# Kernel optimization log

Hardware: AMD Instinct MI355X
Metric: run time of the kernel (lower is better)

## Reference

```python
import jax, jax.numpy as jnp
import numpy as np

H = 768          # hidden_size
V = 512          # vocab_size
NUM_OPS = 64
N_INT = 2        # num_internal_ops
D = 13           # tree depth; complete binary tree
N_NODES = (1 << (D + 1)) - 1  # 16383, level-major layout: level d occupies [2^d-1, 2^(d+1)-1)
TEMP = 3.0


def setup_inputs() -> dict:
    key = jax.random.key(0)
    ks = jax.random.split(key, 24)
    s = 0.02
    nrm = lambda k, shp: jax.random.normal(k, shp, dtype=jnp.float32) * s
    return {
        "ids": jax.random.randint(ks[0], (N_NODES,), 0, V, dtype=jnp.int32),
        "mask": jax.random.randint(ks[1], (N_NODES, NUM_OPS), 0, 2, dtype=jnp.int32),
        # binary Tree-LSTM (N=2), Tai et al. N-ary formulation
        "Wb_iou": nrm(ks[2], (V, 3 * H)), "Ub_iou": nrm(ks[3], (2, H, 3 * H)), "bb_iou": jnp.zeros((3 * H,), jnp.float32),
        "Wb_f": nrm(ks[4], (V, H)), "Ub_f": nrm(ks[5], (2, 2, H, H)), "bb_f": jnp.ones((H,), jnp.float32),
        # ternary Tree-LSTM (N=3)
        "Wt_iou": nrm(ks[6], (V, 3 * H)), "Ut_iou": nrm(ks[7], (3, H, 3 * H)), "bt_iou": jnp.zeros((3 * H,), jnp.float32),
        "Wt_f": nrm(ks[8], (V, H)), "Ut_f": nrm(ks[9], (3, 3, H, H)), "bt_f": jnp.ones((H,), jnp.float32),
        # FFN(H,H,H,n_layers=1): Linear->ReLU->Linear
        "ffn_W1": nrm(ks[10], (H, H)), "ffn_b1": jnp.zeros((H,), jnp.float32),
        "ffn_W2": nrm(ks[11], (H, H)), "ffn_b2": jnp.zeros((H,), jnp.float32),
        # actor heads
        "hl_W": nrm(ks[12], (H, 2)), "hl_b": jnp.zeros((2,), jnp.float32),
        "int_W": nrm(ks[13], (H, N_INT)), "int_b": jnp.zeros((N_INT,), jnp.float32),
        "act_W": nrm(ks[14], (H, NUM_OPS)), "act_b": jnp.zeros((NUM_OPS,), jnp.float32),
    }


def _cell(x_iou, x_f, hc, cc, U_iou, b_iou, U_f, b_f):
    """Batched N-ary Tree-LSTM cell. hc, cc: (n, K, H)."""
    iou = x_iou + jnp.einsum('nkh,kho->no', hc, U_iou) + b_iou
    i, o, g = jnp.split(iou, 3, axis=-1)
    i = jax.nn.sigmoid(i); o = jax.nn.sigmoid(o); g = jnp.tanh(g)
    # per-child forget gate mixes all children hiddens
    f = jax.nn.sigmoid(x_f[:, None, :] + jnp.einsum('nlh,klho->nko', hc, U_f) + b_f)
    c = i * g + jnp.sum(f * cc, axis=1)
    h = o * jnp.tanh(c)
    return h, c


def reference(ids, mask,
              Wb_iou, Ub_iou, bb_iou, Wb_f, Ub_f, bb_f,
              Wt_iou, Ut_iou, bt_iou, Wt_f, Ut_f, bt_f,
              ffn_W1, ffn_b1, ffn_W2, ffn_b2,
              hl_W, hl_b, int_W, int_b, act_W, act_b):
    dt = Wb_iou.dtype
    # ---- apply_binary_lstm: bottom-up, batched per tree level ----
    h_lv = [None] * (D + 1)
    c_lv = [None] * (D + 1)
    for d in range(D, -1, -1):
        n = 1 << d
        off = n - 1
        lid = ids[off:off + n]
        if d == D:  # leaves: missing children -> zero hidden/cell (self.tz)
            hc = jnp.zeros((n, 2, H), dt); cc = jnp.zeros((n, 2, H), dt)
        else:
            hc = h_lv[d + 1].reshape(n, 2, H)
            cc = c_lv[d + 1].reshape(n, 2, H)
        h_lv[d], c_lv[d] = _cell(Wb_iou[lid], Wb_f[lid], hc, cc, Ub_iou, bb_iou, Ub_f, bb_f)
    # ---- internal op 1: apply_ternary_lstm(depth=0) at every node, batched ----
    # uses (own h, child-a h, child-b h); leaves get all zeros (a is None branch)
    h3_parts = []
    for d in range(D + 1):
        n = 1 << d
        off = n - 1
        lid = ids[off:off + n]
        if d == D:
            hc = jnp.zeros((n, 3, H), dt); cc = jnp.zeros((n, 3, H), dt)
        else:
            hc = jnp.concatenate([h_lv[d][:, None, :], h_lv[d + 1].reshape(n, 2, H)], axis=1)
            cc = jnp.concatenate([c_lv[d][:, None, :], c_lv[d + 1].reshape(n, 2, H)], axis=1)
        h3, _ = _cell(Wt_iou[lid], Wt_f[lid], hc, cc, Ut_iou, bt_iou, Ut_f, bt_f)
        h3_parts.append(h3)
    h = jnp.concatenate(h3_parts, axis=0)  # [N_NODES, H], level-major
    # ---- internal op 0: apply_ffn ----
    h = jax.nn.relu(h @ ffn_W1 + ffn_b1) @ ffn_W2 + ffn_b2
    # ---- policy heads (temperature softmaxes, masked actor) ----
    hl = jax.nn.softmax((h @ hl_W + hl_b) / TEMP, axis=-1)
    il = jax.nn.softmax((h @ int_W + int_b) / TEMP, axis=-1)
    mf = mask.astype(dt)
    lin = (h @ act_W + act_b) * mf                       # F.linear with mask-zeroed W, b
    logits = jnp.where(mf > 0, lin, jnp.asarray(-1e30, dt))  # validity_mask.log() + lin
    ap = jax.nn.softmax(logits / TEMP, axis=-1)
    return jnp.concatenate([hl, il, ap], axis=-1)  # [N_NODES, 2 + N_INT + NUM_OPS]
```

## Files before the change

kernel.cpp:

```cpp
#include <hip/hip_runtime.h>
#include <hip/hip_bf16.h>

#define HD 768
#define N_NODES 16383
#define NLEAF_OFF 8191
#define NHF 12582144
#define TEMP 3.0f

using bf16 = __hip_bfloat16;
typedef __attribute__((ext_vector_type(8))) short bf16x8;
typedef __attribute__((ext_vector_type(4))) float f32x4;

__device__ __forceinline__ float sigm(float x) { return 1.0f / (1.0f + __expf(-x)); }
__device__ __forceinline__ float b2f(bf16 v)   { return __bfloat162float(v); }
__device__ __forceinline__ bf16  f2b(float v)  { return __float2bfloat16(v); }

__device__ __forceinline__ void gload16(const void* g, void* l) {
    __builtin_amdgcn_global_load_lds(
        (const __attribute__((address_space(1))) unsigned int*)g,
        (__attribute__((address_space(3))) unsigned int*)l, 16, 0, 0);
}

#define T1SZ 5898240
#define T2SZ 10616832
#define WSZ  589824

__global__ __launch_bounds__(256) void tconv_k(
    const float* __restrict__ Ub_iou, const float* __restrict__ Ub_f,
    const float* __restrict__ Ut_iou, const float* __restrict__ Ut_f,
    const float* __restrict__ ffn_W1,
    bf16* __restrict__ BT1, bf16* __restrict__ BT2, bf16* __restrict__ W1T)
{
    int t = blockIdx.x;
    const float* src; bf16* dst; int C, S, kt, nt;
    if (t < 3456) {
        src = Ub_iou; dst = BT1; C = 2304; S = 1536;
        kt = t % 48; nt = t / 48;
    } else if (t < 5760) {
        int u = t - 3456; int piece = u / 576; u -= piece * 576;
        int kk = piece >> 1, l = piece & 1;
        src = Ub_f + (size_t)(kk * 2 + l) * WSZ;
        dst = BT1 + (size_t)(2304 + kk * 768) * 1536 + l * 768;
        C = 768; S = 1536; kt = u % 24; nt = u / 24;
    } else if (t < 10944) {
        int u = t - 5760;
        src = Ut_iou; dst = BT2; C = 2304; S = 2304;
        kt = u % 72; nt = u / 72;
    } else if (t < 16128) {
        int u = t - 10944; int piece = u / 576; u -= piece * 576;
        int kk = piece / 3, l = piece - kk * 3;
        src = Ut_f + (size_t)(kk * 3 + l) * WSZ;
        dst = BT2 + (size_t)(2304 + kk * 768) * 2304 + l * 768;
        C = 768; S = 2304; kt = u % 24; nt = u / 24;
    } else {
        int u = t - 16128;
        src = ffn_W1; dst = W1T; C = 768; S = 768;
        kt = u % 24; nt = u / 24;
    }
    int k0 = kt * 32, n0 = nt * 32;

    __shared__ float tl[32][33];
    int rr = threadIdx.x >> 5, c = threadIdx.x & 31;
#pragma unroll
    for (int r = 0; r < 32; r += 8)
        tl[rr + r][c] = src[(size_t)(k0 + rr + r) * C + n0 + c];
    __syncthreads();
#pragma unroll
    for (int r = 0; r < 32; r += 8)
        dst[(size_t)(n0 + rr + r) * S + k0 + c] = f2b(tl[c][rr + r]);
}

#define HSZ2 98304
__global__ __launch_bounds__(256) void misc_k(
    const float* __restrict__ hlW, const float* __restrict__ intW,
    const float* __restrict__ actW, const float* __restrict__ W2,
    bf16* __restrict__ WhT, bf16* __restrict__ W2b)
{
    int idx = blockIdx.x * 256 + threadIdx.x;
    if (idx < HSZ2) {
        int n = idx / 768, j = idx - n * 768;
        float v = 0.f;
        if (n < 2)       v = hlW[(size_t)j * 2 + n];
        else if (n < 4)  v = intW[(size_t)j * 2 + (n - 2)];
        else if (n < 68) v = actW[(size_t)j * 64 + (n - 4)];
        WhT[idx] = f2b(v);
    } else if (idx < HSZ2 + WSZ) {
        int i2 = idx - HSZ2;
        W2b[i2] = f2b(W2[i2]);
    }
}

__global__ __launch_bounds__(128) void bck_k(
    const float* __restrict__ b2,
    const float* __restrict__ hlW, const float* __restrict__ hlb,
    const float* __restrict__ intW, const float* __restrict__ intb,
    const float* __restrict__ actW, const float* __restrict__ actb,
    float* __restrict__ bc)
{
    int n = threadIdx.x;
    float s = 0.f;
    for (int j = 0; j < 768; ++j) {
        float wh = 0.f;
        if (n < 2)       wh = hlW[(size_t)j * 2 + n];
        else if (n < 4)  wh = intW[(size_t)j * 2 + (n - 2)];
        else if (n < 68) wh = actW[(size_t)j * 64 + (n - 4)];
        s = fmaf(b2[j], wh, s);
    }
    float hb = 0.f;
    if (n < 2)       hb = hlb[n];
    else if (n < 4)  hb = intb[n - 2];
    else if (n < 68) hb = actb[n - 4];
    bc[n] = s + hb;
}

__global__ __launch_bounds__(256) void vocab_k(
    const float* __restrict__ Wb, const float* __restrict__ bb,
    const float* __restrict__ Wt, const float* __restrict__ bt,
    bf16* __restrict__ Vh, bf16* __restrict__ Vc, bf16* __restrict__ Vh3)
{
    int idx = blockIdx.x * 256 + threadIdx.x;
    if (idx >= 512 * HD) return;
    int id = idx / HD, j = idx - id * HD;
    const float* w = Wb + (size_t)id * 3 * HD;
    float iv = sigm(w[j] + bb[j]);
    float ov = sigm(w[HD + j] + bb[HD + j]);
    float gv = tanhf(w[2 * HD + j] + bb[2 * HD + j]);
    float c = iv * gv;
    Vh[idx] = f2b(ov * tanhf(c));
    Vc[idx] = f2b(c);

    const float* w2 = Wt + (size_t)id * 3 * HD;
    float iv2 = sigm(w2[j] + bt[j]);
    float ov2 = sigm(w2[HD + j] + bt[HD + j]);
    float gv2 = tanhf(w2[2 * HD + j] + bt[2 * HD + j]);
    float c2 = iv2 * gv2;
    Vh3[idx] = f2b(ov2 * tanhf(c2));
}

__global__ __launch_bounds__(256) void lscat_k(
    const int* __restrict__ ids,
    const bf16* __restrict__ Vh, const bf16* __restrict__ Vc,
    const bf16* __restrict__ Vh3,
    bf16* __restrict__ h_all, bf16* __restrict__ c_all, bf16* __restrict__ h3_all)
{
    int idx = blockIdx.x * 256 + threadIdx.x;
    if (idx >= 8192 * 96) return;
    int i = idx / 96, j8 = (idx - i * 96) * 8;
    int g = NLEAF_OFF + i;
    size_t so = (size_t)ids[g] * HD + j8;
    size_t dof = (size_t)g * HD + j8;
    *(uint4*)(h_all + dof)  = *(const uint4*)(Vh + so);
    *(uint4*)(c_all + dof)  = *(const uint4*)(Vc + so);
    *(uint4*)(h3_all + dof) = *(const uint4*)(Vh3 + so);
}

template <int GATHER>
__global__ __launch_bounds__(512, 2) void mm8_k(
    const bf16* __restrict__ A, const bf16* __restrict__ BT,
    bf16* __restrict__ Cb, int M, int N, int K, int NBX)
{
    __shared__ short Al[2][16384];
    __shared__ short Bl[2][16384];

    const int tid  = threadIdx.x;
    const int lane = tid & 63;
    const int wid  = tid >> 6;
    const int wr = wid >> 2, wc = wid & 3;
    const int NT = K >> 6;

    int T = gridDim.x, L = blockIdx.x;
    int q = T >> 3, r = T & 7;
    int xcd = L & 7, i8 = L >> 3;
    int v = (xcd < r ? xcd * (q + 1) : r * (q + 1) + (xcd - r) * q) + i8;
    const int bx = v % NBX, by = v / NBX;

    const int srow = wid * 8 + (lane >> 3);
    const int scol = ((lane & 7) ^ (lane >> 3)) * 8;
    const int frow = lane & 15;
    const int fq   = lane >> 4;

    f32x4 acc[8][4] = {};

    auto stageA = [&](int t, int cr) {
        int slot = t & 1;
        int grow = by * 256 + cr + srow;
        if (grow > M - 1) grow = M - 1;
        int kb = t * 64;
        const bf16* src;
        if constexpr (GATHER) {
            int ch = kb / 768;
            int node = (ch == 0) ? grow : (2 * grow + ch);
            src = A + (size_t)node * 768 + (kb - ch * 768) + scol;
        } else {
            src = A + (size_t)grow * K + kb + scol;
        }
        gload16(src, &Al[slot][(cr + wid * 8) * 64]);
    };
    auto stageB = [&](int t, int cr) {
        int slot = t & 1;
        const bf16* src = BT + (size_t)(bx * 256 + cr + srow) * K + t * 64 + scol;
        gload16(src, &Bl[slot][(cr + wid * 8) * 64]);
    };

    stageB(0, 0);   stageB(0, 64);
    stageB(0, 128); stageB(0, 192);
    stageA(0, 0);   stageA(0, 128);
    stageA(0, 64);  stageA(0, 192);
    stageB(1, 0);   stageB(1, 64);
    stageB(1, 128); stageB(1, 192);
    stageA(1, 0);   stageA(1, 128);
    asm volatile("s_waitcnt vmcnt(6)" ::: "memory");
    __builtin_amdgcn_s_barrier();

#define PHASE(Q, STAGES, TAILWAIT)                                           \
    {                                                                        \
        bf16x8 a[2][2];                                                      \
        _Pragma("unroll")                                                    \
        for (int mq = 0; mq < 2; ++mq)                                       \
            _Pragma("unroll")                                                \
            for (int ks = 0; ks < 2; ++ks)                                   \
                a[mq][ks] = *(const bf16x8*)&Ax[                             \
                    (wr * 128 + ((Q) * 2 + mq) * 16 + frow) * 64             \
                    + (((ks * 4 + fq) ^ (frow & 7)) * 8)];                   \
        STAGES;                                                              \
        __builtin_amdgcn_s_barrier();                                        \
        asm volatile("s_waitcnt lgkmcnt(0)" ::: "memory");                   \
        __builtin_amdgcn_sched_barrier(0);                                   \
        __builtin_amdgcn_s_setprio(1);                                       \
        _Pragma("unroll")                                                    \
        for (int mq = 0; mq < 2; ++mq)                                       \
            _Pragma("unroll")                                                \
            for (int nf = 0; nf < 4; ++nf)                                   \
                _Pragma("unroll")                                            \
                for (int ks = 0; ks < 2; ++ks)                               \
                    acc[(Q) * 2 + mq][nf] =                                  \
                        __builtin_amdgcn_mfma_f32_16x16x32_bf16(             \
                            a[mq][ks], b[nf][ks], acc[(Q) * 2 + mq][nf], 0, 0, 0); \
        __builtin_amdgcn_s_setprio(0);                                       \
        TAILWAIT;                                                            \
        __builtin_amdgcn_s_barrier();                                        \
    }

    for (int t = 0; t < NT; ++t) {
        short* Ax = Al[t & 1];
        short* Bx = Bl[t & 1];
        bf16x8 b[4][2];
#pragma unroll
        for (int nf = 0; nf < 4; ++nf)
#pragma unroll
            for (int ks = 0; ks < 2; ++ks)
                b[nf][ks] = *(const bf16x8*)&Bx[
                    (wc * 64 + nf * 16 + frow) * 64
                    + (((ks * 4 + fq) ^ (frow & 7)) * 8)];

        PHASE(0,
              { if (t + 1 < NT) { stageA(t + 1, 64); stageA(t + 1, 192); } },
              {})
        PHASE(1,
              { if (t + 2 < NT) { stageB(t + 2, 0); stageB(t + 2, 64); } },
              {})
        PHASE(2,
              { if (t + 2 < NT) { stageB(t + 2, 128); stageB(t + 2, 192); } },
              {})
        PHASE(3,
              { if (t + 2 < NT) { stageA(t + 2, 0); stageA(t + 2, 128); } },
              {
                  if (t + 2 < NT) asm volatile("s_waitcnt vmcnt(6)" ::: "memory");
                  else            asm volatile("s_waitcnt vmcnt(0)" ::: "memory");
              })
    }
#undef PHASE

#pragma unroll
    for (int mf = 0; mf < 8; ++mf) {
#pragma unroll
        for (int r2 = 0; r2 < 4; ++r2) {
            int row = by * 256 + wr * 128 + mf * 16 + (lane >> 4) * 4 + r2;
            if (row >= M) continue;
#pragma unroll
            for (int nf = 0; nf < 4; ++nf) {
                int col = bx * 256 + wc * 64 + nf * 16 + (lane & 15);
                Cb[(size_t)row * N + col] = f2b(acc[mf][nf][r2]);
            }
        }
    }
}

template <int EPI, int GATHER>
__global__ __launch_bounds__(256) void mm_k(
    const bf16* __restrict__ A, const bf16* __restrict__ BT,
    float* __restrict__ Cf, bf16* __restrict__ Cb,
    const float* __restrict__ bias,
    int M, int N, int Kc, int Kfull)
{
    __shared__ short As[128 * 32];
    __shared__ short Bs[128 * 32];

    int tid  = threadIdx.x;
    int lane = tid & 63;
    int wave = tid >> 6;
    int wr = wave >> 1, wc = wave & 1;
    int bx = blockIdx.x, by = blockIdx.y;
    int colbase = blockIdx.z * Kc;
    if constexpr (EPI == 0) Cf += (size_t)blockIdx.z * ((size_t)M * N);

    f32x4 acc[4][4] = {};

    int sr  = lane >> 2;
    int sc8 = (lane & 3) * 8;
    int arow0 = by * 128 + wave * 16 + sr;
    int arow1 = arow0 + 64;
    if (arow0 > M - 1) arow0 = M - 1;
    if (arow1 > M - 1) arow1 = M - 1;
    const bf16* gA0 = A + (size_t)arow0 * Kfull + colbase + sc8;
    const bf16* gA1 = A + (size_t)arow1 * Kfull + colbase + sc8;
    const bf16* gB0 = BT + (size_t)(bx * 128 + wave * 16 + sr) * Kfull + colbase + sc8;
    const bf16* gB1 = BT + (size_t)(bx * 128 + wave * 16 + sr + 64) * Kfull + colbase + sc8;
    short* lA0 = As + wave * 512;
    short* lA1 = As + wave * 512 + 2048;
    short* lB0 = Bs + wave * 512;
    short* lB1 = Bs + wave * 512 + 2048;

    int fr = lane & 15;
    int fk = (lane >> 4) << 3;
    const short* pAf = As + (wr * 64 + fr) * 32 + fk;
    const short* pBf = Bs + (wc * 64 + fr) * 32 + fk;

    for (int kt = 0; kt < Kc; kt += 32) {
        if constexpr (GATHER) {
            int abs0 = colbase + kt;
            int ch = (abs0 >= 768) + (abs0 >= 1536);
            int col = abs0 - ch * 768 + sc8;
            int n0 = (ch == 0) ? arow0 : (2 * arow0 + ch);
            int n1 = (ch == 0) ? arow1 : (2 * arow1 + ch);
            gload16(A + (size_t)n0 * HD + col, lA0);
            gload16(A + (size_t)n1 * HD + col, lA1);
        } else {
            gload16(gA0 + kt, lA0);
            gload16(gA1 + kt, lA1);
        }
        gload16(gB0 + kt, lB0);
        gload16(gB1 + kt, lB1);
        __syncthreads();

        bf16x8 a[4], b[4];
#pragma unroll
        for (int m = 0; m < 4; m++) a[m] = *(const bf16x8*)(pAf + m * 512);
#pragma unroll
        for (int n = 0; n < 4; n++) b[n] = *(const bf16x8*)(pBf + n * 512);
#pragma unroll
        for (int m = 0; m < 4; m++)
#pragma unroll
            for (int n = 0; n < 4; n++)
                acc[m][n] = __builtin_amdgcn_mfma_f32_16x16x32_bf16(
                    a[m], b[n], acc[m][n], 0, 0, 0);
        __syncthreads();
    }

    int rbase = by * 128 + wr * 64 + ((lane >> 4) << 2);
    int cbase = bx * 128 + wc * 64 + fr;
#pragma unroll
    for (int m = 0; m < 4; m++) {
#pragma unroll
        for (int r = 0; r < 4; r++) {
            int row = rbase + m * 16 + r;
            if (row >= M) continue;
#pragma unroll
            for (int n = 0; n < 4; n++) {
                int col = cbase + n * 16;
                float v = acc[m][n][r];
                if constexpr (EPI == 1) {
                    v = fmaxf(v + bias[col], 0.f);
                    Cb[(size_t)row * N + col] = f2b(v);
                } else if constexpr (EPI == 3) {
                    Cb[(size_t)row * N + col] = f2b(v);
                } else {
                    Cf[(size_t)row * N + col] = v;
                }
            }
        }
    }
}

__global__ __launch_bounds__(256) void cell1_k(
    const int* __restrict__ ids, const bf16* __restrict__ S,
    const float* __restrict__ Wiou, const float* __restrict__ biou,
    const float* __restrict__ Wf, const float* __restrict__ bfv,
    bf16* __restrict__ h_all, bf16* __restrict__ c_all,
    int m, int offAbs)
{
    int idx = blockIdx.x * blockDim.x + threadIdx.x;
    if (idx >= m * HD) return;
    int i = idx / HD, j = idx - i * HD;
    int g = offAbs + i;
    int id = ids[g];
    const bf16* s = S + (size_t)i * 3840;
    const float* w = Wiou + (size_t)id * 2304;
    float iv = sigm(b2f(s[j]) + w[j] + biou[j]);
    float ov = sigm(b2f(s[HD + j]) + w[HD + j] + biou[HD + j]);
    float gv = tanhf(b2f(s[2 * HD + j]) + w[2 * HD + j] + biou[2 * HD + j]);
    float xf = Wf[(size_t)id * HD + j] + bfv[j];
    float f0 = sigm(b2f(s[3 * HD + j]) + xf);
    float f1 = sigm(b2f(s[4 * HD + j]) + xf);
    float c = iv * gv
            + f0 * b2f(c_all[(size_t)(2 * g + 1) * HD + j])
            + f1 * b2f(c_all[(size_t)(2 * g + 2) * HD + j]);
    h_all[(size_t)g * HD + j] = f2b(ov * tanhf(c));
    c_all[(size_t)g * HD + j] = f2b(c);
}

__global__ __launch_bounds__(256) void cell1s_k(
    const int* __restrict__ ids, const float* __restrict__ Sf,
    const float* __restrict__ Wiou, const float* __restrict__ biou,
    const float* __restrict__ Wf, const float* __restrict__ bfv,
    bf16* __restrict__ h_all, bf16* __restrict__ c_all,
    int m, int offAbs, int KS)
{
    int idx = blockIdx.x * blockDim.x + threadIdx.x;
    if (idx >= m * HD) return;
    int i = idx / HD, j = idx - i * HD;
    int g = offAbs + i;
    int id = ids[g];
    const float* s = Sf + (size_t)i * 3840;
    size_t zs = (size_t)m * 3840;
    float si = 0.f, so = 0.f, su = 0.f, p0 = 0.f, p1 = 0.f;
    for (int z = 0; z < KS; ++z) {
        const float* sz = s + z * zs;
        si += sz[j];
        so += sz[HD + j];
        su += sz[2 * HD + j];
        p0 += sz[3 * HD + j];
        p1 += sz[4 * HD + j];
    }
    const float* w = Wiou + (size_t)id * 2304;
    float iv = sigm(si + w[j] + biou[j]);
    float ov = sigm(so + w[HD + j] + biou[HD + j]);
    float gv = tanhf(su + w[2 * HD + j] + biou[2 * HD + j]);
    float xf = Wf[(size_t)id * HD + j] + bfv[j];
    float f0 = sigm(p0 + xf);
    float f1 = sigm(p1 + xf);
    float c = iv * gv
            + f0 * b2f(c_all[(size_t)(2 * g + 1) * HD + j])
            + f1 * b2f(c_all[(size_t)(2 * g + 2) * HD + j]);
    h_all[(size_t)g * HD + j] = f2b(ov * tanhf(c));
    c_all[(size_t)g * HD + j] = f2b(c);
}

__global__ __launch_bounds__(256) void cell2_k(
    const int* __restrict__ ids, const bf16* __restrict__ S,
    const float* __restrict__ Wiou, const float* __restrict__ biou,
    const float* __restrict__ Wf, const float* __restrict__ bfv,
    const bf16* __restrict__ c_all, bf16* __restrict__ h3_all,
    int m, int g0)
{
    int idx = blockIdx.x * blockDim.x + threadIdx.x;
    if (idx >= m * HD) return;
    int i = idx / HD, j = idx - i * HD;
    int g = g0 + i;
    int id = ids[g];
    const bf16* s = S + (size_t)i * 4608;
    const float* w = Wiou + (size_t)id * 2304;
    float iv = sigm(b2f(s[j]) + w[j] + biou[j]);
    float ov = sigm(b2f(s[HD + j]) + w[HD + j] + biou[HD + j]);
    float gv = tanhf(b2f(s[2 * HD + j]) + w[2 * HD + j] + biou[2 * HD + j]);
    float xf = Wf[(size_t)id * HD + j] + bfv[j];
    float f0 = sigm(b2f(s[3 * HD + j]) + xf);
    float f1 = sigm(b2f(s[4 * HD + j]) + xf);
    float f2 = sigm(b2f(s[5 * HD + j]) + xf);
    float c = iv * gv
            + f0 * b2f(c_all[(size_t)g * HD + j])
            + f1 * b2f(c_all[(size_t)(2 * g + 1) * HD + j])
            + f2 * b2f(c_all[(size_t)(2 * g + 2) * HD + j]);
    h3_all[(size_t)g * HD + j] = f2b(ov * tanhf(c));
}

__global__ __launch_bounds__(256) void hsm_k(
    const float* __restrict__ L, const int* __restrict__ mask,
    const float* __restrict__ bc, float* __restrict__ out)
{
    int g = blockIdx.x * 4 + (threadIdx.x >> 6);
    if (g >= N_NODES) return;
    int t = threadIdx.x & 63;
    const float* lr = L + (size_t)g * 128;

    bool on = mask[(size_t)g * 64 + t] > 0;
    float x = (lr[4 + t] + bc[4 + t]) * (1.0f / TEMP);
    float mx = on ? x : -INFINITY;
#pragma unroll
    for (int o = 32; o; o >>= 1) mx = fmaxf(mx, __shfl_xor(mx, o));
    float e = on ? __expf(x - mx) : 0.0f;
    float s = e;
#pragma unroll
    for (int o = 32; o; o >>= 1) s += __shfl_xor(s, o);
    float r = (s > 0.f) ? e / s : (1.0f / 64.0f);
    out[(size_t)g * 68 + 4 + t] = r;

    if (t == 0) {
        float a = (lr[0] + bc[0]) * (1.0f / TEMP);
        float b = (lr[1] + bc[1]) * (1.0f / TEMP);
        float m2 = fmaxf(a, b);
        float e0 = __expf(a - m2), e1 = __expf(b - m2);
        out[(size_t)g * 68 + 0] = e0 / (e0 + e1);
        out[(size_t)g * 68 + 1] = e1 / (e0 + e1);
    } else if (t == 1) {
        float a = (lr[2] + bc[2]) * (1.0f / TEMP);
        float b = (lr[3] + bc[3]) * (1.0f / TEMP);
        float m2 = fmaxf(a, b);
        float e0 = __expf(a - m2), e1 = __expf(b - m2);
        out[(size_t)g * 68 + 2] = e0 / (e0 + e1);
        out[(size_t)g * 68 + 3] = e1 / (e0 + e1);
    }
}

extern "C" void kernel_launch(void* const* d_in, const int* in_sizes, int n_in,
                              void* d_out, int out_size, void* d_ws, size_t ws_size,
                              hipStream_t stream)
{
    const int*   ids     = (const int*)d_in[0];
    const int*   mask    = (const int*)d_in[1];
    const float* Wb_iou  = (const float*)d_in[2];
    const float* Ub_iou  = (const float*)d_in[3];
    const float* bb_iou  = (const float*)d_in[4];
    const float* Wb_f    = (const float*)d_in[5];
    const float* Ub_f    = (const float*)d_in[6];
    const float* bb_f    = (const float*)d_in[7];
    const float* Wt_iou  = (const float*)d_in[8];
    const float* Ut_iou  = (const float*)d_in[9];
    const float* bt_iou  = (const float*)d_in[10];
    const float* Wt_f    = (const float*)d_in[11];
    const float* Ut_f    = (const float*)d_in[12];
    const float* bt_f    = (const float*)d_in[13];
    const float* ffn_W1  = (const float*)d_in[14];
    const float* ffn_b1  = (const float*)d_in[15];
    const float* ffn_W2  = (const float*)d_in[16];
    const float* ffn_b2  = (const float*)d_in[17];
    const float* hl_W    = (const float*)d_in[18];
    const float* hl_b    = (const float*)d_in[19];
    const float* int_W   = (const float*)d_in[20];
    const float* int_b   = (const float*)d_in[21];
    const float* act_W   = (const float*)d_in[22];
    const float* act_b   = (const float*)d_in[23];

    char* p = (char*)d_ws;
    bf16* h_all  = (bf16*)p; p += (size_t)NHF * 2;
    bf16* c_all  = (bf16*)p; p += (size_t)NHF * 2;
    bf16* h3_all = (bf16*)p; p += (size_t)NHF * 2;
    bf16* BT1 = (bf16*)p; p += (size_t)T1SZ * 2;
    bf16* BT2 = (bf16*)p; p += (size_t)T2SZ * 2;
    bf16* W1T = (bf16*)p; p += (size_t)WSZ * 2;
    bf16* WcT = (bf16*)p; p += (size_t)128 * 768 * 2;
    bf16* WhT = (bf16*)p; p += (size_t)HSZ2 * 2;
    bf16* W2b = (bf16*)p; p += (size_t)WSZ * 2;
    bf16* Vh  = (bf16*)p; p += (size_t)512 * HD * 2;
    bf16* Vc  = (bf16*)p; p += (size_t)512 * HD * 2;
    bf16* Vh3 = (bf16*)p; p += (size_t)512 * HD * 2;
    float* bc = (float*)p; p += 512;
    bf16* Sb  = (bf16*)p;
    float* Sf = (float*)Sb;
    bf16* t1  = c_all;
    float* Lg = (float*)h3_all;

    tconv_k<<<16704, 256, 0, stream>>>(
        Ub_iou, Ub_f, Ut_iou, Ut_f, ffn_W1, BT1, BT2, W1T);
    misc_k<<<(HSZ2 + WSZ + 255) / 256, 256, 0, stream>>>(
        hl_W, int_W, act_W, ffn_W2, WhT, W2b);
    bck_k<<<1, 128, 0, stream>>>(
        ffn_b2, hl_W, hl_b, int_W, int_b, act_W, act_b, bc);
    mm_k<3, 0><<<dim3(6, 1), 256, 0, stream>>>(
        WhT, W2b, nullptr, WcT, nullptr, 128, 768, 768, 768);

    vocab_k<<<(512 * HD + 255) / 256, 256, 0, stream>>>(
        Wb_iou, bb_iou, Wt_iou, bt_iou, Vh, Vc, Vh3);
    lscat_k<<<(8192 * 96 + 255) / 256, 256, 0, stream>>>(
        ids, Vh, Vc, Vh3, h_all, c_all, h3_all);

    for (int d = 12; d >= 0; --d) {
        int n = 1 << d;
        int childoff = 2 * n - 1;
        if (n >= 2048) {
            mm8_k<0><<<15 * (n / 256), 512, 0, stream>>>(
                h_all + (size_t)childoff * HD, BT1, Sb, n, 3840, 1536, 15);
            cell1_k<<<(n * HD + 255) / 256, 256, 0, stream>>>(
                ids, Sb, Wb_iou, bb_iou, Wb_f, bb_f, h_all, c_all, n, n - 1);
        } else if (n >= 512) {
            mm_k<3, 0><<<dim3(30, n / 128), 256, 0, stream>>>(
                h_all + (size_t)childoff * HD, BT1, nullptr, Sb, nullptr,
                n, 3840, 1536, 1536);
            cell1_k<<<(n * HD + 255) / 256, 256, 0, stream>>>(
                ids, Sb, Wb_iou, bb_iou, Wb_f, bb_f, h_all, c_all, n, n - 1);
        } else {
            mm_k<0, 0><<<dim3(30, (n + 127) / 128, 6), 256, 0, stream>>>(
                h_all + (size_t)childoff * HD, BT1, Sf, nullptr, nullptr,
                n, 3840, 256, 1536);
            cell1s_k<<<(n * HD + 255) / 256, 256, 0, stream>>>(
                ids, Sf, Wb_iou, bb_iou, Wb_f, bb_f, h_all, c_all, n, n - 1, 6);
        }
    }

    mm8_k<1><<<18 * 32, 512, 0, stream>>>(
        h_all, BT2, Sb, NLEAF_OFF, 4608, 2304, 18);
    cell2_k<<<(NLEAF_OFF * HD + 255) / 256, 256, 0, stream>>>(
        ids, Sb, Wt_iou, bt_iou, Wt_f, bt_f, c_all, h3_all, NLEAF_OFF, 0);

    mm_k<1, 0><<<dim3(6, 128), 256, 0, stream>>>(
        h3_all, W1T, nullptr, t1, ffn_b1, N_NODES, 768, 768, 768);

    mm_k<0, 0><<<dim3(1, 128), 256, 0, stream>>>(
        t1, WcT, Lg, nullptr, nullptr, N_NODES, 128, 768, 768);
    hsm_k<<<(N_NODES + 3) / 4, 256, 0, stream>>>(
        Lg, mask, bc, (float*)d_out);
}
```

Baseline: 783.0 us.

## Fuse small tree levels into one cooperative persistent kernel with grid syncs

Levels 8 down to 0 of the binary Tree-LSTM sweep now run inside a single cooperative kernel. It computes a split-K MFMA GEMM straight from global memory, calls grid.sync, applies the cell update, and syncs again before the next level. This replaces around 18 small kernel launches that each did little work, so launch overhead and gaps between dependent kernels are meant to go away. In exchange the GEMM path is simpler and has no LDS tiling, only 120 blocks run, and every level pays two grid-wide barriers.

```diff
diff --git a/kernel.cpp b/kernel.cpp
--- a/kernel.cpp
+++ b/kernel.cpp
@@ -1,5 +1,8 @@
 #include <hip/hip_runtime.h>
 #include <hip/hip_bf16.h>
+#include <hip/hip_cooperative_groups.h>
+
+namespace cg = cooperative_groups;
 
 #define HD 768
 #define N_NODES 16383
@@ -152,6 +155,91 @@
     *(uint4*)(h_all + dof)  = *(const uint4*)(Vh + so);
     *(uint4*)(c_all + dof)  = *(const uint4*)(Vc + so);
     *(uint4*)(h3_all + dof) = *(const uint4*)(Vh3 + so);
+}
+
+__global__ __launch_bounds__(512) void tail_k(
+    const int* __restrict__ ids,
+    bf16* __restrict__ h_all, bf16* __restrict__ c_all,
+    const bf16* __restrict__ BT1,
+    const float* __restrict__ Wiou, const float* __restrict__ biou,
+    const float* __restrict__ Wf, const float* __restrict__ bfv,
+    float* __restrict__ Sf)
+{
+    cg::grid_group grid = cg::this_grid();
+    const int lane = threadIdx.x & 63;
+    const int gw = (blockIdx.x * 512 + threadIdx.x) >> 6;
+    const int gt = blockIdx.x * 512 + threadIdx.x;
+
+    const int fr = lane & 15;
+    const int fk = (lane >> 4) << 3;
+
+    for (int d = 8; d >= 0; --d) {
+        const int n = 1 << d, off = n - 1, childoff = 2 * n - 1;
+        const bf16* A = h_all + (size_t)childoff * HD;
+        const int rowTiles = (n + 15) >> 4;
+        const int tilesPerZ = rowTiles * 60;
+        const int tiles = tilesPerZ * 2;
+
+        for (int t = gw; t < tiles; t += 960) {
+            int z = t / tilesPerZ;
+            int rem = t - z * tilesPerZ;
+            int rt = rem / 60, ct = rem - rt * 60;
+            int r0 = rt * 16, c0 = ct * 64;
+            int arow = r0 + fr;
+            if (arow > n - 1) arow = n - 1;
+            const bf16* Ap = A + (size_t)arow * 1536 + z * 768 + fk;
+            const bf16* Bp0 = BT1 + (size_t)(c0 + fr) * 1536 + z * 768 + fk;
+
+            f32x4 acc[4] = {};
+            for (int kt = 0; kt < 768; kt += 32) {
+                bf16x8 av = *(const bf16x8*)(Ap + kt);
+#pragma unroll
+                for (int f = 0; f < 4; ++f) {
+                    bf16x8 bv = *(const bf16x8*)(Bp0 + (size_t)f * 16 * 1536 + kt);
+                    acc[f] = __builtin_amdgcn_mfma_f32_16x16x32_bf16(
+                        av, bv, acc[f], 0, 0, 0);
+                }
+            }
+            int drow = r0 + ((lane >> 4) << 2);
+#pragma unroll
+            for (int f = 0; f < 4; ++f)
+#pragma unroll
+                for (int r = 0; r < 4; ++r) {
+                    int row = drow + r;
+                    if (row < n)
+                        Sf[((size_t)z * 256 + row) * 3840 + c0 + f * 16 + fr] =
+                            acc[f][r];
+                }
+        }
+        grid.sync();
+
+        int tot = n * HD;
+        for (int idx = gt; idx < tot; idx += 61440) {
+            int i = idx / HD, j = idx - i * HD;
+            int g = off + i;
+            int id = ids[g];
+            const float* s0 = Sf + (size_t)i * 3840;
+            const float* s1 = Sf + (size_t)(256 + i) * 3840;
+            float si = s0[j] + s1[j];
+            float so = s0[768 + j] + s1[768 + j];
+            float su = s0[1536 + j] + s1[1536 + j];
+            float p0 = s0[2304 + j] + s1[2304 + j];
+            float p1 = s0[3072 + j] + s1[3072 + j];
+            const float* w = Wiou + (size_t)id * 2304;
+            float iv = sigm(si + w[j] + biou[j]);
+            float ov = sigm(so + w[768 + j] + biou[768 + j]);
+            float gv = tanhf(su + w[1536 + j] + biou[1536 + j]);
+            float xf = Wf[(size_t)id * HD + j] + bfv[j];
+            float f0 = sigm(p0 + xf);
+            float f1 = sigm(p1 + xf);
+            float c = iv * gv
+                    + f0 * b2f(c_all[(size_t)(2 * g + 1) * HD + j])
+                    + f1 * b2f(c_all[(size_t)(2 * g + 2) * HD + j]);
+            h_all[(size_t)g * HD + j] = f2b(ov * tanhf(c));
+            c_all[(size_t)g * HD + j] = f2b(c);
+        }
+        if (d > 0) grid.sync();
+    }
 }
 
 template <int GATHER>
@@ -409,43 +497,6 @@
     c_all[(size_t)g * HD + j] = f2b(c);
 }
 
-__global__ __launch_bounds__(256) void cell1s_k(
-    const int* __restrict__ ids, const float* __restrict__ Sf,
-    const float* __restrict__ Wiou, const float* __restrict__ biou,
-    const float* __restrict__ Wf, const float* __restrict__ bfv,
-    bf16* __restrict__ h_all, bf16* __restrict__ c_all,
-    int m, int offAbs, int KS)
-{
-    int idx = blockIdx.x * blockDim.x + threadIdx.x;
-    if (idx >= m * HD) return;
-    int i = idx / HD, j = idx - i * HD;
-    int g = offAbs + i;
-    int id = ids[g];
-    const float* s = Sf + (size_t)i * 3840;
-    size_t zs = (size_t)m * 3840;
-    float si = 0.f, so = 0.f, su = 0.f, p0 = 0.f, p1 = 0.f;
-    for (int z = 0; z < KS; ++z) {
-        const float* sz = s + z * zs;
-        si += sz[j];
-        so += sz[HD + j];
-        su += sz[2 * HD + j];
-        p0 += sz[3 * HD + j];
-        p1 += sz[4 * HD + j];
-    }
-    const float* w = Wiou + (size_t)id * 2304;
-    float iv = sigm(si + w[j] + biou[j]);
-    float ov = sigm(so + w[HD + j] + biou[HD + j]);
-    float gv = tanhf(su + w[2 * HD + j] + biou[2 * HD + j]);
-    float xf = Wf[(size_t)id * HD + j] + bfv[j];
-    float f0 = sigm(p0 + xf);
-    float f1 = sigm(p1 + xf);
-    float c = iv * gv
-            + f0 * b2f(c_all[(size_t)(2 * g + 1) * HD + j])
-            + f1 * b2f(c_all[(size_t)(2 * g + 2) * HD + j]);
-    h_all[(size_t)g * HD + j] = f2b(ov * tanhf(c));
-    c_all[(size_t)g * HD + j] = f2b(c);
-}
-
 __global__ __launch_bounds__(256) void cell2_k(
     const int* __restrict__ ids, const bf16* __restrict__ S,
     const float* __restrict__ Wiou, const float* __restrict__ biou,
@@ -574,27 +625,29 @@
     lscat_k<<<(8192 * 96 + 255) / 256, 256, 0, stream>>>(
         ids, Vh, Vc, Vh3, h_all, c_all, h3_all);
 
-    for (int d = 12; d >= 0; --d) {
+    for (int d = 12; d >= 9; --d) {
         int n = 1 << d;
         int childoff = 2 * n - 1;
         if (n >= 2048) {
             mm8_k<0><<<15 * (n / 256), 512, 0, stream>>>(
                 h_all + (size_t)childoff * HD, BT1, Sb, n, 3840, 1536, 15);
-            cell1_k<<<(n * HD + 255) / 256, 256, 0, stream>>>(
-                ids, Sb, Wb_iou, bb_iou, Wb_f, bb_f, h_all, c_all, n, n - 1);
-        } else if (n >= 512) {
+        } else {
             mm_k<3, 0><<<dim3(30, n / 128), 256, 0, stream>>>(
                 h_all + (size_t)childoff * HD, BT1, nullptr, Sb, nullptr,
                 n, 3840, 1536, 1536);
-            cell1_k<<<(n * HD + 255) / 256, 256, 0, stream>>>(
-                ids, Sb, Wb_iou, bb_iou, Wb_f, bb_f, h_all, c_all, n, n - 1);
-        } else {
-            mm_k<0, 0><<<dim3(30, (n + 127) / 128, 6), 256, 0, stream>>>(
-                h_all + (size_t)childoff * HD, BT1, Sf, nullptr, nullptr,
-                n, 3840, 256, 1536);
-            cell1s_k<<<(n * HD + 255) / 256, 256, 0, stream>>>(
-                ids, Sf, Wb_iou, bb_iou, Wb_f, bb_f, h_all, c_all, n, n - 1, 6);
         }
+        cell1_k<<<(n * HD + 255) / 256, 256, 0, stream>>>(
+            ids, Sb, Wb_iou, bb_iou, Wb_f, bb_f, h_all, c_all, n, n - 1);
+    }
+
+    {
+        void* args[] = {
+            (void*)&ids, (void*)&h_all, (void*)&c_all, (void*)&BT1,
+            (void*)&Wb_iou, (void*)&bb_iou, (void*)&Wb_f, (void*)&bb_f,
+            (void*)&Sf
+        };
+        hipLaunchCooperativeKernel((void*)tail_k, dim3(120), dim3(512),
+                                   args, 0, stream);
     }
 
     mm8_k<1><<<18 * 32, 512, 0, stream>>>(
```

New measurement: 1.181 ms. 50.8% more time.
